# Kernel tuning notes

Hardware: AMD Instinct MI355X
Metric: run time of the kernel (lower is better)

Reference implementation:

```python
import jax, jax.numpy as jnp
import numpy as np

DIM = 1024
NUM_EXPERTS = 8
TOP_K = 2
B, S = 2, 2048
HID = 4 * DIM


def setup_inputs() -> dict:
    key = jax.random.key(0)
    ks = jax.random.split(key, 7)
    scale = 0.02
    x = jax.random.normal(ks[0], (B, S, DIM), dtype=jnp.float32)
    gate_w = jax.random.normal(ks[1], (DIM, NUM_EXPERTS), dtype=jnp.float32) * scale
    gate_b = jnp.zeros((NUM_EXPERTS,), dtype=jnp.float32)
    w1 = jax.random.normal(ks[2], (NUM_EXPERTS, DIM, HID), dtype=jnp.float32) * scale
    b1 = jnp.zeros((NUM_EXPERTS, HID), dtype=jnp.float32)
    w2 = jax.random.normal(ks[3], (NUM_EXPERTS, HID, DIM), dtype=jnp.float32) * scale
    b2 = jnp.zeros((NUM_EXPERTS, DIM), dtype=jnp.float32)
    return {"x": x, "gate_w": gate_w, "gate_b": gate_b,
            "w1": w1, "b1": b1, "w2": w2, "b2": b2}


def reference(x, gate_w, gate_b, w1, b1, w2, b2):
    # Gate: [B,S,E]
    gates = jnp.einsum('bsd,de->bse', x, gate_w) + gate_b
    top_w, top_idx = jax.lax.top_k(gates, TOP_K)          # [B,S,K]
    probs = jax.nn.softmax(top_w, axis=-1)                # softmax over selected logits
    # Dense all-expert FFN (matches original: every expert runs on every token)
    h = jnp.einsum('bsd,edh->bseh', x, w1) + b1           # [B,S,E,4D]
    h = jax.nn.gelu(h, approximate=False)                 # exact GELU (torch default)
    y = jnp.einsum('bseh,ehd->bsed', h, w2) + b2          # [B,S,E,D]
    # Select top-k experts per token and combine
    sel = jnp.take_along_axis(y, top_idx[..., None], axis=2)   # [B,S,K,D]
    return jnp.sum(sel * probs[..., None], axis=2)        # [B,S,D]
```

## Files before the change

### kernel.cpp

```cpp
#include <hip/hip_runtime.h>
#include <hip/hip_bf16.h>

#define T_TOKENS 4096
#define DIM      1024
#define HID      4096
#define NE       8
#define CAP      4096
#define SPLITS   4
#define KSP      (HID / SPLITS)

typedef __attribute__((ext_vector_type(8))) short  bf16x8;
typedef __attribute__((ext_vector_type(4))) float  f32x4;
typedef __attribute__((ext_vector_type(4))) ushort u16x4;

__device__ static inline ushort f2bf(float f) {
    __hip_bfloat16 h = __float2bfloat16(f);
    return *(ushort*)&h;
}

__device__ static inline void gll16(const void* g, void* l) {
    __builtin_amdgcn_global_load_lds(
        (const __attribute__((address_space(1))) void*)g,
        (__attribute__((address_space(3))) void*)l,
        16, 0, 0);
}

#define MFMA16(a, b, c) __builtin_amdgcn_mfma_f32_16x16x32_bf16((a), (b), (c), 0, 0, 0)

__global__ __launch_bounds__(64) void gate_kernel(
    const float* __restrict__ x, const float* __restrict__ gw,
    const float* __restrict__ gb, __hip_bfloat16* __restrict__ xb,
    int* __restrict__ counts, int* __restrict__ tlist, float* __restrict__ plist)
{
    const int tok = blockIdx.x;
    const int l   = threadIdx.x;
    const float* xr = x + (size_t)tok * DIM;

    float part[NE];
#pragma unroll
    for (int e = 0; e < NE; e++) part[e] = 0.f;

#pragma unroll
    for (int i = 0; i < DIM / 64; i++) {
        int d = i * 64 + l;
        float xv = xr[d];
        xb[(size_t)tok * DIM + d] = __float2bfloat16(xv);
        const float4* g4 = (const float4*)(gw + (size_t)d * NE);
        float4 a = g4[0], b = g4[1];
        part[0] += xv * a.x; part[1] += xv * a.y;
        part[2] += xv * a.z; part[3] += xv * a.w;
        part[4] += xv * b.x; part[5] += xv * b.y;
        part[6] += xv * b.z; part[7] += xv * b.w;
    }
#pragma unroll
    for (int off = 32; off > 0; off >>= 1) {
#pragma unroll
        for (int e = 0; e < NE; e++) part[e] += __shfl_xor(part[e], off, 64);
    }
    if (l == 0) {
        float lg[NE];
#pragma unroll
        for (int e = 0; e < NE; e++) lg[e] = part[e] + gb[e];
        int i0 = 0;
#pragma unroll
        for (int e = 1; e < NE; e++) if (lg[e] > lg[i0]) i0 = e;
        int i1 = (i0 == 0) ? 1 : 0;
#pragma unroll
        for (int e = 0; e < NE; e++) if (e != i0 && lg[e] > lg[i1]) i1 = e;
        float t  = expf(lg[i1] - lg[i0]);
        float p0 = 1.f / (1.f + t);
        float p1 = t / (1.f + t);
        int pos0 = atomicAdd(&counts[i0], 1);
        tlist[i0 * CAP + pos0] = tok;              plist[i0 * CAP + pos0] = p0;
        int pos1 = atomicAdd(&counts[i1], 1);
        tlist[i1 * CAP + pos1] = tok | (1 << 15);  plist[i1 * CAP + pos1] = p1;
    }
}

__global__ void finalize_kernel(const int* __restrict__ counts, int* __restrict__ base)
{
    if (threadIdx.x == 0) {
        int acc = 0;
        for (int e = 0; e < NE; e++) { base[e] = acc; acc += counts[e]; }
        base[NE] = acc;
    }
}

__global__ __launch_bounds__(256) void transpose_cvt64(
    const float* __restrict__ in, __hip_bfloat16* __restrict__ outp, int K, int N)
{
    __shared__ ushort tile[64][68];
    const int e  = blockIdx.z;
    const float* src = in + (size_t)e * K * N;
    ushort* dst = (ushort*)outp + (size_t)e * K * N;
    const int k0 = blockIdx.y * 64, n0 = blockIdx.x * 64;
    const int tid = threadIdx.x;

    const int rn4 = (tid & 15) * 4;
    const int rk  = tid >> 4;
#pragma unroll
    for (int p = 0; p < 4; p++) {
        int k = rk + p * 16;
        float4 v = *(const float4*)&src[(size_t)(k0 + k) * N + n0 + rn4];
        tile[k][rn4 + 0] = f2bf(v.x);
        tile[k][rn4 + 1] = f2bf(v.y);
        tile[k][rn4 + 2] = f2bf(v.z);
        tile[k][rn4 + 3] = f2bf(v.w);
    }
    __syncthreads();
    const int wk4 = (tid & 15) * 4;
    const int wn  = tid >> 4;
#pragma unroll
    for (int p = 0; p < 4; p++) {
        int n = wn + p * 16;
        u16x4 u;
        u[0] = tile[wk4 + 0][n];
        u[1] = tile[wk4 + 1][n];
        u[2] = tile[wk4 + 2][n];
        u[3] = tile[wk4 + 3][n];
        *(u16x4*)&dst[(size_t)(n0 + n) * K + k0 + wk4] = u;
    }
}


#define MFMA_ALL                                                             \
    _Pragma("unroll")                                                        \
    for (int mi = 0; mi < 4; mi++)                                           \
        _Pragma("unroll")                                                    \
        for (int nj = 0; nj < 4; nj++)                                       \
            acc[mi][nj] = MFMA16(af[mi], bfr[nj], acc[mi][nj]);

#define GEMM_CORE(NK, srcA0, srcA1, srcB0, srcB1)                            \
    f32x4 acc[4][4];                                                         \
    _Pragma("unroll")                                                        \
    for (int i = 0; i < 4; i++)                                              \
        _Pragma("unroll")                                                    \
        for (int j = 0; j < 4; j++) acc[i][j] = (f32x4){0.f,0.f,0.f,0.f};    \
    gll16(srcA0, &lds[lo0]);        gll16(srcA1, &lds[lo1]);                 \
    gll16(srcB0, &lds[8192 + lo0]); gll16(srcB1, &lds[8192 + lo1]);          \
    int cur = 0;                                                             \
    _Pragma("unroll 1")                                                      \
    for (int ks = 0; ks < NK; ks++) {                                        \
        __syncthreads();                                                     \
        if (ks + 1 < NK) {                                                   \
            const int ko = (ks + 1) * 32;                                    \
            const int nb = (cur ^ 1) * 4096;                                 \
            gll16(srcA0 + ko, &lds[nb + lo0]);                               \
            gll16(srcA1 + ko, &lds[nb + lo1]);                               \
            gll16(srcB0 + ko, &lds[8192 + nb + lo0]);                        \
            gll16(srcB1 + ko, &lds[8192 + nb + lo1]);                        \
        }                                                                    \
        const int cb_ = cur * 4096;                                          \
        bf16x8 af[4], bfr[4];                                                \
        _Pragma("unroll")                                                    \
        for (int mi = 0; mi < 4; mi++) {                                     \
            int row = wr * 64 + mi * 16 + lm;                                \
            af[mi] = *(const bf16x8*)&lds[cb_ + row * 32 + rch];             \
        }                                                                    \
        _Pragma("unroll")                                                    \
        for (int nj = 0; nj < 4; nj++) {                                     \
            int row = wc * 64 + nj * 16 + lm;                                \
            bfr[nj] = *(const bf16x8*)&lds[8192 + cb_ + row * 32 + rch];     \
        }                                                                    \
        MFMA_ALL                                                             \
        cur ^= 1;                                                            \
    }

#define CORE_IDX                                                             \
    const int tid = threadIdx.x;                                             \
    const int l = tid & 63, w = tid >> 6;                                    \
    const int wr = w >> 1, wc = w & 1;                                       \
    const int lm = l & 15, kg = l >> 4;                                      \
    const int rch = (kg ^ ((lm >> 1) & 3)) * 8;                              \
    const int slot0 = w * 128 + l;                                           \
    const int slot1 = w * 128 + 64 + l;                                      \
    const int row0 = slot0 >> 2, row1 = slot1 >> 2;                          \
    const int ch0 = ((slot0 & 3) ^ ((row0 >> 1) & 3)) * 8;                   \
    const int ch1 = ((slot1 & 3) ^ ((row1 >> 1) & 3)) * 8;                   \
    const int lo0 = w * 1024;                                                \
    const int lo1 = w * 1024 + 512;

__global__ __launch_bounds__(256, 3) void ffn1_kernel(
    const __hip_bfloat16* __restrict__ xb, const __hip_bfloat16* __restrict__ w1t,
    const float* __restrict__ b1, const int* __restrict__ counts,
    const int* __restrict__ base, const int* __restrict__ tlist,
    int* __restrict__ tickets, __hip_bfloat16* __restrict__ H)
{
    __shared__ __align__(16) ushort lds[16384];
    __shared__ int s_task;
    CORE_IDX
    const int e  = blockIdx.x & 7;
    const int ne = counts[e];
    const int mt = (ne + 127) >> 7;
    const int ntask = mt * 32;
    const int hb = base[e];
    if (mt == 0) return;

    for (;;) {
        __syncthreads();
        if (tid == 0) s_task = atomicAdd(&tickets[e], 1);
        __syncthreads();
        const int i = s_task;
        if (i >= ntask) break;
        const int cb = i / mt, rb = i - cb * mt;

        const int r0g = rb * 128 + row0;
        const int r1g = rb * 128 + row1;
        const int tok0 = tlist[e * CAP + (r0g < ne ? r0g : ne - 1)] & 0xFFF;
        const int tok1 = tlist[e * CAP + (r1g < ne ? r1g : ne - 1)] & 0xFFF;
        const ushort* srcA0 = (const ushort*)xb + (size_t)tok0 * DIM + ch0;
        const ushort* srcA1 = (const ushort*)xb + (size_t)tok1 * DIM + ch1;
        const ushort* srcB0 = (const ushort*)w1t + ((size_t)e * HID + cb * 128 + row0) * DIM + ch0;
        const ushort* srcB1 = (const ushort*)w1t + ((size_t)e * HID + cb * 128 + row1) * DIM + ch1;

        GEMM_CORE(32, srcA0, srcA1, srcB0, srcB1)

        __syncthreads();
#pragma unroll
        for (int nj = 0; nj < 4; nj++) {
            int col = wc * 64 + nj * 16 + lm;
            float bias = b1[e * HID + cb * 128 + col];
#pragma unroll
            for (int mi = 0; mi < 4; mi++) {
#pragma unroll
                for (int jj = 0; jj < 4; jj++) {
                    int row = wr * 64 + mi * 16 + kg * 4 + jj;
                    float vv = acc[mi][nj][jj] + bias;
                    vv = 0.5f * vv * (1.0f + erff(vv * 0.70710678118654752f));
                    lds[row * 128 + (col ^ ((row & 12) << 2))] = f2bf(vv);
                }
            }
        }
        __syncthreads();
#pragma unroll
        for (int pch = 0; pch < 8; pch++) {
            int c   = pch * 256 + tid;
            int row = c >> 4, seg = c & 15;
            int r   = rb * 128 + row;
            if (r < ne) {
                int pseg = seg ^ ((row & 12) >> 1);
                bf16x8 vv8 = *(const bf16x8*)&lds[row * 128 + pseg * 8];
                *(bf16x8*)((ushort*)H + (size_t)(hb + r) * HID + cb * 128 + seg * 8) = vv8;
            }
        }
    }
}

__global__ __launch_bounds__(256, 3) void ffn2_kernel(
    const __hip_bfloat16* __restrict__ H, const __hip_bfloat16* __restrict__ w2t,
    const float* __restrict__ b2, const int* __restrict__ counts,
    const int* __restrict__ base, const int* __restrict__ tlist,
    const float* __restrict__ plist, int* __restrict__ tickets,
    __hip_bfloat16* __restrict__ Y)
{
    __shared__ __align__(16) ushort lds[16384];
    __shared__ int s_task;
    CORE_IDX
    const int e  = blockIdx.x & 7;
    const int ne = counts[e];
    const int mt = (ne + 127) >> 7;
    const int ntask = mt * 32;
    const int hb = base[e];
    if (mt == 0) return;

    for (;;) {
        __syncthreads();
        if (tid == 0) s_task = atomicAdd(&tickets[NE + e], 1);
        __syncthreads();
        const int i = s_task;
        if (i >= ntask) break;
        const int c  = i / mt, rb = i - c * mt;
        const int sp = c >> 3, cb = c & 7;

        const int r0g = rb * 128 + row0;
        const int r1g = rb * 128 + row1;
        const int hr0 = hb + (r0g < ne ? r0g : ne - 1);
        const int hr1 = hb + (r1g < ne ? r1g : ne - 1);
        const size_t ko0 = (size_t)sp * KSP;
        const ushort* srcA0 = (const ushort*)H + (size_t)hr0 * HID + ko0 + ch0;
        const ushort* srcA1 = (const ushort*)H + (size_t)hr1 * HID + ko0 + ch1;
        const ushort* srcB0 = (const ushort*)w2t + ((size_t)e * DIM + cb * 128 + row0) * HID + ko0 + ch0;
        const ushort* srcB1 = (const ushort*)w2t + ((size_t)e * DIM + cb * 128 + row1) * HID + ko0 + ch1;

        GEMM_CORE(32, srcA0, srcA1, srcB0, srcB1)

        __syncthreads();
#pragma unroll
        for (int nj = 0; nj < 4; nj++) {
            int col = wc * 64 + nj * 16 + lm;
            float bias = (sp == 0) ? b2[e * DIM + cb * 128 + col] : 0.f;
#pragma unroll
            for (int mi = 0; mi < 4; mi++) {
#pragma unroll
                for (int jj = 0; jj < 4; jj++) {
                    int row = wr * 64 + mi * 16 + kg * 4 + jj;
                    int r   = rb * 128 + row;
                    float p = plist[e * CAP + (r < ne ? r : ne - 1)];
                    float vv = (acc[mi][nj][jj] + bias) * p;
                    lds[row * 128 + (col ^ ((row & 12) << 2))] = f2bf(vv);
                }
            }
        }
        __syncthreads();
#pragma unroll
        for (int pch = 0; pch < 8; pch++) {
            int cch = pch * 256 + tid;
            int row = cch >> 4, seg = cch & 15;
            int r   = rb * 128 + row;
            if (r < ne) {
                int tv  = tlist[e * CAP + r];
                int tok = tv & 0xFFF, kk = tv >> 15;
                int pseg = seg ^ ((row & 12) >> 1);
                bf16x8 vv8 = *(const bf16x8*)&lds[row * 128 + pseg * 8];
                *(bf16x8*)((ushort*)Y + ((size_t)(kk * 4 + sp) * T_TOKENS + tok) * DIM
                           + cb * 128 + seg * 8) = vv8;
            }
        }
    }
}

__global__ __launch_bounds__(256) void reduce_kernel(
    const __hip_bfloat16* __restrict__ Y, float* __restrict__ out)
{
    const size_t i = ((size_t)blockIdx.x * 256 + threadIdx.x) * 8;
    float s[8];
#pragma unroll
    for (int j = 0; j < 8; j++) s[j] = 0.f;
#pragma unroll
    for (int sl = 0; sl < 8; sl++) {
        bf16x8 v = *(const bf16x8*)((const ushort*)Y + (size_t)sl * T_TOKENS * DIM + i);
#pragma unroll
        for (int j = 0; j < 8; j++) {
            union { unsigned int ui; float f; } cv;
            cv.ui = ((unsigned int)(ushort)v[j]) << 16;
            s[j] += cv.f;
        }
    }
#pragma unroll
    for (int j = 0; j < 8; j++) out[i + j] = s[j];
}

extern "C" void kernel_launch(void* const* d_in, const int* in_sizes, int n_in,
                              void* d_out, int out_size, void* d_ws, size_t ws_size,
                              hipStream_t stream)
{
    const float* x  = (const float*)d_in[0];
    const float* gw = (const float*)d_in[1];
    const float* gb = (const float*)d_in[2];
    const float* w1 = (const float*)d_in[3];
    const float* b1 = (const float*)d_in[4];
    const float* w2 = (const float*)d_in[5];
    const float* b2 = (const float*)d_in[6];
    float* out = (float*)d_out;

    char* ws = (char*)d_ws;
    __hip_bfloat16* w1t = (__hip_bfloat16*)(ws);
    __hip_bfloat16* w2t = (__hip_bfloat16*)(ws + 67108864);
    __hip_bfloat16* Hb  = (__hip_bfloat16*)(ws + 134217728);
    __hip_bfloat16* xb  = (__hip_bfloat16*)(ws + 201326592);
    int*   tlist  = (int*)  (ws + 209715200);
    float* plist  = (float*)(ws + 209846272);
    int*   counts = (int*)  (ws + 209977344);
    int*   basep  = (int*)  (ws + 209977408);
    int*   tickets= (int*)  (ws + 209977472);
    __hip_bfloat16* Y = (__hip_bfloat16*)(ws);

    hipMemsetAsync(counts, 0, 192, stream);

    gate_kernel<<<T_TOKENS, 64, 0, stream>>>(x, gw, gb, xb, counts, tlist, plist);
    finalize_kernel<<<1, 64, 0, stream>>>(counts, basep);

    transpose_cvt64<<<dim3(HID / 64, DIM / 64, NE), 256, 0, stream>>>(w1, w1t, DIM, HID);
    transpose_cvt64<<<dim3(DIM / 64, HID / 64, NE), 256, 0, stream>>>(w2, w2t, HID, DIM);

    ffn1_kernel<<<768, 256, 0, stream>>>(
        xb, w1t, b1, counts, basep, tlist, tickets, Hb);
    ffn2_kernel<<<768, 256, 0, stream>>>(
        Hb, w2t, b2, counts, basep, tlist, plist, tickets, Y);
    reduce_kernel<<<(T_TOKENS * DIM / 8) / 256, 256, 0, stream>>>(Y, out);
}
```

Before: 435.6 us.

## Fold w2 transpose-convert into ffn1 persistent blocks as tail work

Drops the standalone w2 transpose/bf16 conversion kernel and has each persistent ffn1 block, once its expert's GEMM tasks run out, take 64x64 tiles of w2 from a new per-expert ticket counter and transpose/convert them. This hides the w2 conversion in the ffn1 tail and saves a launch. Ticket indices shift (ffn2 now uses tickets[2*NE+e]) and the memset grows to cover the extra counters. The w1 transpose is specialised to constant dims and its LDS pad changes from 68 to 70.

```diff
diff --git a/kernel.cpp b/kernel.cpp
--- a/kernel.cpp
+++ b/kernel.cpp
@@ -86,13 +86,13 @@
     }
 }
 
-__global__ __launch_bounds__(256) void transpose_cvt64(
-    const float* __restrict__ in, __hip_bfloat16* __restrict__ outp, int K, int N)
-{
-    __shared__ ushort tile[64][68];
+__global__ __launch_bounds__(256) void transpose_w1(
+    const float* __restrict__ in, __hip_bfloat16* __restrict__ outp)
+{
+    __shared__ ushort tile[64][70];
     const int e  = blockIdx.z;
-    const float* src = in + (size_t)e * K * N;
-    ushort* dst = (ushort*)outp + (size_t)e * K * N;
+    const float* src = in + (size_t)e * DIM * HID;
+    ushort* dst = (ushort*)outp + (size_t)e * DIM * HID;
     const int k0 = blockIdx.y * 64, n0 = blockIdx.x * 64;
     const int tid = threadIdx.x;
 
@@ -101,7 +101,7 @@
 #pragma unroll
     for (int p = 0; p < 4; p++) {
         int k = rk + p * 16;
-        float4 v = *(const float4*)&src[(size_t)(k0 + k) * N + n0 + rn4];
+        float4 v = *(const float4*)&src[(size_t)(k0 + k) * HID + n0 + rn4];
         tile[k][rn4 + 0] = f2bf(v.x);
         tile[k][rn4 + 1] = f2bf(v.y);
         tile[k][rn4 + 2] = f2bf(v.z);
@@ -118,7 +118,7 @@
         u[1] = tile[wk4 + 1][n];
         u[2] = tile[wk4 + 2][n];
         u[3] = tile[wk4 + 3][n];
-        *(u16x4*)&dst[(size_t)(n0 + n) * K + k0 + wk4] = u;
+        *(u16x4*)&dst[(size_t)(n0 + n) * DIM + k0 + wk4] = u;
     }
 }
 
@@ -182,9 +182,110 @@
 
 __global__ __launch_bounds__(256, 3) void ffn1_kernel(
     const __hip_bfloat16* __restrict__ xb, const __hip_bfloat16* __restrict__ w1t,
-    const float* __restrict__ b1, const int* __restrict__ counts,
+    const float* __restrict__ b1, const float* __restrict__ w2,
+    __hip_bfloat16* __restrict__ w2t, const int* __restrict__ counts,
     const int* __restrict__ base, const int* __restrict__ tlist,
     int* __restrict__ tickets, __hip_bfloat16* __restrict__ H)
+{
+    __shared__ __align__(16) ushort lds[16384];
+    __shared__ int s_task;
+    CORE_IDX
+    const int e  = blockIdx.x & 7;
+    const int ne = counts[e];
+    const int mt = (ne + 127) >> 7;
+    const int ntask = mt * 32;
+    const int hb = base[e];
+
+    if (mt != 0)
+    for (;;) {
+        __syncthreads();
+        if (tid == 0) s_task = atomicAdd(&tickets[e], 1);
+        __syncthreads();
+        const int i = s_task;
+        if (i >= ntask) break;
+        const int cb = i / mt, rb = i - cb * mt;
+
+        const int r0g = rb * 128 + row0;
+        const int r1g = rb * 128 + row1;
+        const int tok0 = tlist[e * CAP + (r0g < ne ? r0g : ne - 1)] & 0xFFF;
+        const int tok1 = tlist[e * CAP + (r1g < ne ? r1g : ne - 1)] & 0xFFF;
+        const ushort* srcA0 = (const ushort*)xb + (size_t)tok0 * DIM + ch0;
+        const ushort* srcA1 = (const ushort*)xb + (size_t)tok1 * DIM + ch1;
+        const ushort* srcB0 = (const ushort*)w1t + ((size_t)e * HID + cb * 128 + row0) * DIM + ch0;
+        const ushort* srcB1 = (const ushort*)w1t + ((size_t)e * HID + cb * 128 + row1) * DIM + ch1;
+
+        GEMM_CORE(32, srcA0, srcA1, srcB0, srcB1)
+
+        __syncthreads();
+#pragma unroll
+        for (int nj = 0; nj < 4; nj++) {
+            int col = wc * 64 + nj * 16 + lm;
+            float bias = b1[e * HID + cb * 128 + col];
+#pragma unroll
+            for (int mi = 0; mi < 4; mi++) {
+#pragma unroll
+                for (int jj = 0; jj < 4; jj++) {
+                    int row = wr * 64 + mi * 16 + kg * 4 + jj;
+                    float vv = acc[mi][nj][jj] + bias;
+                    vv = 0.5f * vv * (1.0f + erff(vv * 0.70710678118654752f));
+                    lds[row * 128 + (col ^ ((row & 12) << 2))] = f2bf(vv);
+                }
+            }
+        }
+        __syncthreads();
+#pragma unroll
+        for (int pch = 0; pch < 8; pch++) {
+            int c   = pch * 256 + tid;
+            int row = c >> 4, seg = c & 15;
+            int r   = rb * 128 + row;
+            if (r < ne) {
+                int pseg = seg ^ ((row & 12) >> 1);
+                bf16x8 vv8 = *(const bf16x8*)&lds[row * 128 + pseg * 8];
+                *(bf16x8*)((ushort*)H + (size_t)(hb + r) * HID + cb * 128 + seg * 8) = vv8;
+            }
+        }
+    }
+
+    const float* wsrc = w2 + (size_t)e * HID * DIM;
+    ushort* wdst = (ushort*)w2t + (size_t)e * HID * DIM;
+    for (;;) {
+        __syncthreads();
+        if (tid == 0) s_task = atomicAdd(&tickets[NE + e], 1);
+        __syncthreads();
+        const int i = s_task;
+        if (i >= 1024) break;
+        const int k0 = (i >> 4) * 64, n0 = (i & 15) * 64;
+        const int rn4 = (tid & 15) * 4, rk = tid >> 4;
+#pragma unroll
+        for (int p = 0; p < 4; p++) {
+            int k = rk + p * 16;
+            float4 v = *(const float4*)&wsrc[(size_t)(k0 + k) * DIM + n0 + rn4];
+            lds[k * 70 + rn4 + 0] = f2bf(v.x);
+            lds[k * 70 + rn4 + 1] = f2bf(v.y);
+            lds[k * 70 + rn4 + 2] = f2bf(v.z);
+            lds[k * 70 + rn4 + 3] = f2bf(v.w);
+        }
+        __syncthreads();
+        const int wk4 = (tid & 15) * 4, wn = tid >> 4;
+#pragma unroll
+        for (int p = 0; p < 4; p++) {
+            int n = wn + p * 16;
+            u16x4 u;
+            u[0] = lds[(wk4 + 0) * 70 + n];
+            u[1] = lds[(wk4 + 1) * 70 + n];
+            u[2] = lds[(wk4 + 2) * 70 + n];
+            u[3] = lds[(wk4 + 3) * 70 + n];
+            *(u16x4*)&wdst[(size_t)(n0 + n) * HID + k0 + wk4] = u;
+        }
+    }
+}
+
+__global__ __launch_bounds__(256, 3) void ffn2_kernel(
+    const __hip_bfloat16* __restrict__ H, const __hip_bfloat16* __restrict__ w2t,
+    const float* __restrict__ b2, const int* __restrict__ counts,
+    const int* __restrict__ base, const int* __restrict__ tlist,
+    const float* __restrict__ plist, int* __restrict__ tickets,
+    __hip_bfloat16* __restrict__ Y)
 {
     __shared__ __align__(16) ushort lds[16384];
     __shared__ int s_task;
@@ -198,74 +299,7 @@
 
     for (;;) {
         __syncthreads();
-        if (tid == 0) s_task = atomicAdd(&tickets[e], 1);
-        __syncthreads();
-        const int i = s_task;
-        if (i >= ntask) break;
-        const int cb = i / mt, rb = i - cb * mt;
-
-        const int r0g = rb * 128 + row0;
-        const int r1g = rb * 128 + row1;
-        const int tok0 = tlist[e * CAP + (r0g < ne ? r0g : ne - 1)] & 0xFFF;
-        const int tok1 = tlist[e * CAP + (r1g < ne ? r1g : ne - 1)] & 0xFFF;
-        const ushort* srcA0 = (const ushort*)xb + (size_t)tok0 * DIM + ch0;
-        const ushort* srcA1 = (const ushort*)xb + (size_t)tok1 * DIM + ch1;
-        const ushort* srcB0 = (const ushort*)w1t + ((size_t)e * HID + cb * 128 + row0) * DIM + ch0;
-        const ushort* srcB1 = (const ushort*)w1t + ((size_t)e * HID + cb * 128 + row1) * DIM + ch1;
-
-        GEMM_CORE(32, srcA0, srcA1, srcB0, srcB1)
-
-        __syncthreads();
-#pragma unroll
-        for (int nj = 0; nj < 4; nj++) {
-            int col = wc * 64 + nj * 16 + lm;
-            float bias = b1[e * HID + cb * 128 + col];
-#pragma unroll
-            for (int mi = 0; mi < 4; mi++) {
-#pragma unroll
-                for (int jj = 0; jj < 4; jj++) {
-                    int row = wr * 64 + mi * 16 + kg * 4 + jj;
-                    float vv = acc[mi][nj][jj] + bias;
-                    vv = 0.5f * vv * (1.0f + erff(vv * 0.70710678118654752f));
-                    lds[row * 128 + (col ^ ((row & 12) << 2))] = f2bf(vv);
-                }
-            }
-        }
-        __syncthreads();
-#pragma unroll
-        for (int pch = 0; pch < 8; pch++) {
-            int c   = pch * 256 + tid;
-            int row = c >> 4, seg = c & 15;
-            int r   = rb * 128 + row;
-            if (r < ne) {
-                int pseg = seg ^ ((row & 12) >> 1);
-                bf16x8 vv8 = *(const bf16x8*)&lds[row * 128 + pseg * 8];
-                *(bf16x8*)((ushort*)H + (size_t)(hb + r) * HID + cb * 128 + seg * 8) = vv8;
-            }
-        }
-    }
-}
-
-__global__ __launch_bounds__(256, 3) void ffn2_kernel(
-    const __hip_bfloat16* __restrict__ H, const __hip_bfloat16* __restrict__ w2t,
-    const float* __restrict__ b2, const int* __restrict__ counts,
-    const int* __restrict__ base, const int* __restrict__ tlist,
-    const float* __restrict__ plist, int* __restrict__ tickets,
-    __hip_bfloat16* __restrict__ Y)
-{
-    __shared__ __align__(16) ushort lds[16384];
-    __shared__ int s_task;
-    CORE_IDX
-    const int e  = blockIdx.x & 7;
-    const int ne = counts[e];
-    const int mt = (ne + 127) >> 7;
-    const int ntask = mt * 32;
-    const int hb = base[e];
-    if (mt == 0) return;
-
-    for (;;) {
-        __syncthreads();
-        if (tid == 0) s_task = atomicAdd(&tickets[NE + e], 1);
+        if (tid == 0) s_task = atomicAdd(&tickets[2 * NE + e], 1);
         __syncthreads();
         const int i = s_task;
         if (i >= ntask) break;
@@ -365,16 +399,15 @@
     int*   tickets= (int*)  (ws + 209977472);
     __hip_bfloat16* Y = (__hip_bfloat16*)(ws);
 
-    hipMemsetAsync(counts, 0, 192, stream);
+    hipMemsetAsync(counts, 0, 256, stream);
 
     gate_kernel<<<T_TOKENS, 64, 0, stream>>>(x, gw, gb, xb, counts, tlist, plist);
     finalize_kernel<<<1, 64, 0, stream>>>(counts, basep);
 
-    transpose_cvt64<<<dim3(HID / 64, DIM / 64, NE), 256, 0, stream>>>(w1, w1t, DIM, HID);
-    transpose_cvt64<<<dim3(DIM / 64, HID / 64, NE), 256, 0, stream>>>(w2, w2t, HID, DIM);
+    transpose_w1<<<dim3(HID / 64, DIM / 64, NE), 256, 0, stream>>>(w1, w1t);
 
     ffn1_kernel<<<768, 256, 0, stream>>>(
-        xb, w1t, b1, counts, basep, tlist, tickets, Hb);
+        xb, w1t, b1, w2, w2t, counts, basep, tlist, tickets, Hb);
     ffn2_kernel<<<768, 256, 0, stream>>>(
         Hb, w2t, b2, counts, basep, tlist, plist, tickets, Y);
     reduce_kernel<<<(T_TOKENS * DIM / 8) / 256, 256, 0, stream>>>(Y, out);
```

After: 473.1 us. 1.09x slower.
